# Optimization experiments

Measured on AMD Instinct MI355X. Metric: run time of the kernel, lower is better.

The kernel has to match this reference:

```python
import jax, jax.numpy as jnp
import numpy as np

_SAMPLING_EPS = 1e-05
_FP16_TINY = float(np.finfo(np.float16).tiny)  # masked_fill value used by the torch code


def _token_mask(tokens, num_seqs, vocab_size):
    # bin-count via scatter-add into width vocab+1 (padding id == vocab), then mask
    rows = jnp.arange(num_seqs)[:, None]
    counts = jnp.zeros((num_seqs, vocab_size + 1), jnp.int32).at[rows, tokens].add(1)
    return counts[:, :vocab_size] > 0


def setup_inputs() -> dict:
    key = jax.random.key(0)
    ks = jax.random.split(key, 9)
    B, V, PL, OL = 128, 128000, 2048, 256
    logits = jax.random.normal(ks[0], (B, V), dtype=jnp.float32) * 4.0
    prompt_tokens = jax.random.randint(ks[1], (B, PL), 0, V, dtype=jnp.int64)
    output_tokens = jax.random.randint(ks[2], (B, OL), 0, V, dtype=jnp.int64)
    presence_penalties = jax.random.uniform(ks[3], (B,), dtype=jnp.float32)
    frequency_penalties = jax.random.uniform(ks[4], (B,), dtype=jnp.float32)
    repetition_penalties = 1.0 + 0.3 * jax.random.uniform(ks[5], (B,), dtype=jnp.float32)
    temperature = 0.1 + 0.9 * jax.random.uniform(ks[6], (B,), dtype=jnp.float32)
    top_k = jax.random.randint(ks[7], (B,), 1, 100, dtype=jnp.int64)
    top_p = 0.5 + 0.49 * jax.random.uniform(ks[8], (B,), dtype=jnp.float32)
    return {
        "logits": logits,
        "prompt_tokens": prompt_tokens,
        "output_tokens": output_tokens,
        "presence_penalties": presence_penalties,
        "frequency_penalties": frequency_penalties,
        "repetition_penalties": repetition_penalties,
        "temperature": temperature,
        "top_k": top_k,
        "top_p": top_p,
    }


def reference(logits, prompt_tokens, output_tokens, presence_penalties,
              frequency_penalties, repetition_penalties, temperature,
              top_k, top_p):
    B, V = logits.shape
    logits = logits.astype(jnp.float32)

    # --- penalties (NOTE: torch code computes frequency counts but never applies
    # frequency_penalties; we faithfully do the same) ---
    prompt_mask = _token_mask(prompt_tokens, B, V)
    output_mask = _token_mask(output_tokens, B, V)
    pen = jnp.where(prompt_mask | output_mask, repetition_penalties[:, None], 1.0)
    logits = jnp.where(logits > 0, logits / pen, logits * pen)
    logits = logits - presence_penalties[:, None] * output_mask.astype(jnp.float32)

    # --- temperature ---
    temp = jnp.where(temperature < _SAMPLING_EPS, 1.0, temperature)
    logits = logits / temp[:, None]

    # --- top-k / top-p via ascending sort (mirrors torch implementation) ---
    idx = jnp.argsort(logits, axis=-1)                      # ascending
    ls = jnp.take_along_axis(logits, idx, axis=-1)
    thr_pos = (V - top_k.astype(jnp.int32))[:, None]
    thr = jnp.take_along_axis(ls, thr_pos, axis=-1)         # [B,1]
    ls = jnp.where(ls < thr, _FP16_TINY, ls)
    probs_sort = jax.nn.softmax(ls, axis=-1)
    csum = jnp.cumsum(probs_sort, axis=-1)
    tp_mask = csum <= (1.0 - top_p)[:, None]
    tp_mask = tp_mask.at[:, -1].set(False)
    ls = jnp.where(tp_mask, _FP16_TINY, ls)

    # unsort back to original vocab order
    rows = jnp.arange(B)[:, None]
    out_logits = jnp.zeros_like(logits).at[rows, idx].set(ls)

    probs = jax.nn.softmax(out_logits, axis=-1)
    return probs, prompt_mask, output_mask
```

## Files before the change

### kernel.cpp

```cpp
#include <hip/hip_runtime.h>
#include <math.h>

#define B   128
#define V   128000
#define WPR 4000
#define PL  2048
#define OL  256
#define BPR 25
#define ITERS 5
#define TLOC 128
#define CAP  6144
#define FP16_TINY 6.103515625e-05f

#define HBINS 4096
#define HIDX(b) ((b) + ((b) >> 4))
#define HSZ (HBINS + (HBINS >> 4))

__device__ __forceinline__ unsigned key_of(float f) {
    unsigned u = __float_as_uint(f);
    unsigned m = (unsigned)(((int)u) >> 31) | 0x80000000u;
    return u ^ m;
}
__device__ __forceinline__ float key_inv(unsigned k) {
    unsigned u = (k & 0x80000000u) ? (k ^ 0x80000000u) : ~k;
    return __uint_as_float(u);
}

__device__ __forceinline__ float xform(float x, int pm, int om,
                                       float rp, float rrp, float pres, float itt) {
#pragma clang fp contract(off)
    float m = (pm | om) ? ((x > 0.0f) ? rrp : rp) : 1.0f;
    float l = x * m;
    if (om) l = l - pres;
    return l * itt;
}

__device__ __forceinline__ unsigned wave_suffix_u(unsigned x, int lane) {
#pragma unroll
    for (int o = 1; o < 64; o <<= 1) {
        unsigned a = __shfl_down(x, o);
        if (lane + o < 64) x += a;
    }
    return x;
}
__device__ __forceinline__ unsigned wave_prefix_u(unsigned x, int lane) {
#pragma unroll
    for (int o = 1; o < 64; o <<= 1) {
        unsigned a = __shfl_up(x, o);
        if (lane >= o) x += a;
    }
    return x;
}
__device__ __forceinline__ double wave_suffix_d(double x, int lane) {
#pragma unroll
    for (int o = 1; o < 64; o <<= 1) {
        double a = __shfl_down(x, o);
        if (lane + o < 64) x += a;
    }
    return x;
}
__device__ __forceinline__ double wave_sum_d(double x) {
#pragma unroll
    for (int o = 1; o < 64; o <<= 1) x += __shfl_xor(x, o);
    return x;
}
__device__ __forceinline__ unsigned wave_sum_u(unsigned x) {
#pragma unroll
    for (int o = 1; o < 64; o <<= 1) x += __shfl_xor(x, o);
    return x;
}

__global__ __launch_bounds__(256) void k_scatter(const int* __restrict__ ptok,
                                                 const int* __restrict__ otok,
                                                 unsigned* __restrict__ bitP,
                                                 unsigned* __restrict__ bitO,
                                                 unsigned* __restrict__ cnt) {
    __shared__ unsigned mp[WPR];
    __shared__ unsigned mo[WPR];
    int r = blockIdx.x;
    int t = threadIdx.x;
    for (int i = t; i < WPR; i += 256) { mp[i] = 0u; mo[i] = 0u; }
    if (t == 0) cnt[r] = 0u;
    __syncthreads();
    const int* prow = ptok + (size_t)r * PL;
    const int* orow = otok + (size_t)r * OL;
    for (int i = t; i < PL; i += 256) {
        int tok = prow[i];
        if ((unsigned)tok < (unsigned)V) atomicOr(&mp[tok >> 5], 1u << (tok & 31));
    }
    for (int i = t; i < OL; i += 256) {
        int tok = orow[i];
        if ((unsigned)tok < (unsigned)V) atomicOr(&mo[tok >> 5], 1u << (tok & 31));
    }
    __syncthreads();
    unsigned* bpo = bitP + (size_t)r * WPR;
    unsigned* boo = bitO + (size_t)r * WPR;
    for (int i = t; i < WPR; i += 256) { bpo[i] = mp[i]; boo[i] = mo[i]; }
}

__global__ __launch_bounds__(256) void k_main(
    const float* __restrict__ logits,
    const unsigned* __restrict__ bitP, const unsigned* __restrict__ bitO,
    const float* __restrict__ rep, const float* __restrict__ pres,
    const float* __restrict__ temp,
    float* __restrict__ outPm, float* __restrict__ outOm,
    unsigned* __restrict__ cnt, unsigned long long* __restrict__ cand)
{
    __shared__ unsigned h[HSZ];
    __shared__ unsigned wsum[4];
    __shared__ int s_beta;
    __shared__ unsigned s_base;
    int r = blockIdx.y;
    int c0 = blockIdx.x * (ITERS * 1024);
    int t = threadIdx.x;
    int lane = t & 63, wid = t >> 6;
    for (int i = t; i < HSZ; i += 256) h[i] = 0u;
    __syncthreads();
    float rp = rep[r], pp = pres[r];
    float tt = temp[r]; tt = (tt < 1e-5f) ? 1.0f : tt;
    float rrp = 1.0f / rp;
    float itt = 1.0f / tt;
    const float* lrow = logits + (size_t)r * V;
    float* pmrow = outPm + (size_t)r * V;
    float* omrow = outOm + (size_t)r * V;
    const unsigned* bp = bitP + (size_t)r * WPR;
    const unsigned* bo = bitO + (size_t)r * WPR;
    uint4 kv4[ITERS];
#pragma unroll
    for (int it = 0; it < ITERS; it++) {
        int i = c0 + it * 1024 + t * 4;
        float4 x = *(const float4*)(lrow + i);
        unsigned wp = bp[i >> 5], wo = bo[i >> 5];
        int sh = i & 31;
        float xs[4] = {x.x, x.y, x.z, x.w};
        unsigned ks[4];
        float fp[4], fo[4];
#pragma unroll
        for (int j = 0; j < 4; j++) {
            int p = (wp >> (sh + j)) & 1;
            int o = (wo >> (sh + j)) & 1;
            float l = xform(xs[j], p, o, rp, rrp, pp, itt);
            unsigned key = key_of(l);
            atomicAdd(&h[HIDX(key >> 20)], 1u);
            ks[j] = key; fp[j] = (float)p; fo[j] = (float)o;
        }
        kv4[it] = make_uint4(ks[0], ks[1], ks[2], ks[3]);
        *(float4*)(pmrow + i) = make_float4(fp[0], fp[1], fp[2], fp[3]);
        *(float4*)(omrow + i) = make_float4(fo[0], fo[1], fo[2], fo[3]);
    }
    __syncthreads();
    unsigned cs = 0;
#pragma unroll
    for (int j = 0; j < 16; j++) cs += h[HIDX(t * 16 + j)];
    unsigned sfx = wave_suffix_u(cs, lane);
    if (lane == 0) wsum[wid] = sfx;
    __syncthreads();
    unsigned suf = sfx;
#pragma unroll
    for (int w2 = 0; w2 < 4; w2++) if (w2 > wid) suf += wsum[w2];
    unsigned Snext = suf - cs;
    if (suf >= TLOC && Snext < TLOC) {
        unsigned run = Snext;
        int beta = t * 16;
        for (int j = 15; j >= 0; j--) {
            run += h[HIDX(t * 16 + j)];
            if (run >= TLOC) { beta = t * 16 + j; break; }
        }
        s_beta = beta;
    }
    __syncthreads();
    unsigned beta = (unsigned)s_beta;
    unsigned myc = 0;
#pragma unroll
    for (int it = 0; it < ITERS; it++) {
        unsigned ks[4] = {kv4[it].x, kv4[it].y, kv4[it].z, kv4[it].w};
#pragma unroll
        for (int j = 0; j < 4; j++)
            if ((ks[j] >> 20) >= beta) myc++;
    }
    unsigned pfx = wave_prefix_u(myc, lane);
    if (lane == 63) wsum[wid] = pfx;
    __syncthreads();
    unsigned pv = pfx;
#pragma unroll
    for (int w2 = 0; w2 < 4; w2++) if (w2 < wid) pv += wsum[w2];
    if (t == 255) s_base = atomicAdd(&cnt[r], pv);
    __syncthreads();
    unsigned w = s_base + (pv - myc);
#pragma unroll
    for (int it = 0; it < ITERS; it++) {
        unsigned ks[4] = {kv4[it].x, kv4[it].y, kv4[it].z, kv4[it].w};
#pragma unroll
        for (int j = 0; j < 4; j++) {
            unsigned key = ks[j];
            if ((key >> 20) >= beta) {
                if (w < (unsigned)CAP) {
                    int idx = c0 + it * 1024 + t * 4 + j;
                    cand[(size_t)r * CAP + w] =
                        ((unsigned long long)key << 32) | (unsigned)idx;
                }
                w++;
            }
        }
    }
}

__global__ __launch_bounds__(256) void k_select(
    const unsigned* __restrict__ cnt, const unsigned long long* __restrict__ cand,
    const int* __restrict__ topk, const float* __restrict__ topp,
    float4* __restrict__ params, int* __restrict__ idxc,
    unsigned* __restrict__ kn, int* __restrict__ kidx, float* __restrict__ kprob)
{
    __shared__ unsigned long long list[CAP];
    __shared__ unsigned long long kv[256];
    __shared__ unsigned rh[256];
    __shared__ double wD[4];
    __shared__ unsigned wU[4];
    __shared__ unsigned s_prefix, s_krem, s_kcnt;
    int r = blockIdx.x;
    int t = threadIdx.x;
    int lane = t & 63, wid = t >> 6;
    int n = (int)min(cnt[r], (unsigned)CAP);
    const unsigned long long* crow = cand + (size_t)r * CAP;
    for (int i = t; i < n; i += 256) list[i] = crow[i];
    int k = topk[r]; k = max(1, min(k, 127));
    if (t == 0) { s_prefix = 0u; s_krem = (unsigned)k; }
    __syncthreads();
    for (int round = 3; round >= 0; round--) {
        int shift = round * 8;
        unsigned prefix = s_prefix;
        unsigned krem = s_krem;
        unsigned maskAbove = (round == 3) ? 0u : (0xFFFFFFFFu << (shift + 8));
        rh[t] = 0u;
        __syncthreads();
        for (int i = t; i < n; i += 256) {
            unsigned key = (unsigned)(list[i] >> 32);
            if ((key & maskAbove) == (prefix & maskAbove))
                atomicAdd(&rh[(key >> shift) & 255u], 1u);
        }
        __syncthreads();
        unsigned vv = rh[t];
        unsigned sfx = wave_suffix_u(vv, lane);
        if (lane == 0) wU[wid] = sfx;
        __syncthreads();
        unsigned suf = sfx;
#pragma unroll
        for (int w2 = 0; w2 < 4; w2++) if (w2 > wid) suf += wU[w2];
        unsigned Sx = suf - vv;
        if (suf >= krem && Sx < krem) {
            s_prefix = prefix | ((unsigned)t << shift);
            s_krem = krem - Sx;
        }
        __syncthreads();
    }
    unsigned thrkey = s_prefix;
    if (t == 0) s_kcnt = 0u;
    __syncthreads();
    for (int i = t; i < n; i += 256) {
        if ((unsigned)(list[i] >> 32) >= thrkey) {
            unsigned pos = atomicAdd(&s_kcnt, 1u);
            if (pos < 256u) kv[pos] = list[i];
        }
    }
    __syncthreads();
    int K = (int)min(s_kcnt, 256u);
    if (t >= K) kv[t] = 0ULL;
    __syncthreads();
    for (unsigned k2 = 2; k2 <= 256; k2 <<= 1) {
        for (unsigned j2 = k2 >> 1; j2 > 0; j2 >>= 1) {
            unsigned ixj = (unsigned)t ^ j2;
            if (ixj > (unsigned)t) {
                unsigned long long a = kv[t], b = kv[ixj];
                bool descBlock = (((unsigned)t & k2) == 0u);
                bool doSwap = descBlock ? (a < b) : (a > b);
                if (doSwap) { kv[t] = b; kv[ixj] = a; }
            }
            __syncthreads();
        }
    }
    float Mxf = key_inv((unsigned)(kv[0] >> 32));
    double MxD = (double)Mxf;
    double e_t = (t < K) ? exp((double)key_inv((unsigned)(kv[t] >> 32)) - MxD)
                         : 0.0;
    double red = wave_sum_d(e_t);
    if (lane == 0) wD[wid] = red;
    __syncthreads();
    double S = wD[0] + wD[1] + wD[2] + wD[3];
    __syncthreads();
    double sv = wave_suffix_d(e_t, lane);
    if (lane == 0) wD[wid] = sv;
    __syncthreads();
    double suf_t = sv;
#pragma unroll
    for (int w2 = 0; w2 < 4; w2++) if (w2 > wid) suf_t += wD[w2];
    double e_tinyD = exp((double)FP16_TINY - MxD);
    double Z1 = (double)(V - K) * e_tinyD + S;
    double base = (double)(V - K) * e_tinyD / Z1;
    double thresh = 1.0 - (double)topp[r];
    unsigned flag = (t >= 1 && t < K && (base + suf_t / Z1) <= thresh) ? 1u : 0u;
    unsigned fr = wave_sum_u(flag);
    if (lane == 0) wU[wid] = fr;
    __syncthreads();
    int cm = (int)(wU[0] + wU[1] + wU[2] + wU[3]);
    int ns = K - cm;
    __syncthreads();
    double e2 = (t < ns) ? e_t : 0.0;
    double r2 = wave_sum_d(e2);
    if (lane == 0) wD[wid] = r2;
    __syncthreads();
    double S2 = wD[0] + wD[1] + wD[2] + wD[3];
    unsigned bkey = (unsigned)(kv[ns - 1] >> 32);
    float v_b = key_inv(bkey);
    float tiny_e = expf(FP16_TINY - Mxf);
    double Z2 = (double)(V - ns) * (double)tiny_e + S2;
    float invZ2 = (float)(1.0 / Z2);
    if (t == 0) {
        params[r] = make_float4(v_b, Mxf, invZ2, tiny_e * invZ2);
        idxc[r] = (int)(kv[ns - 1] & 0xFFFFFFFFu);
        kn[r] = (unsigned)ns;
    }
    if (t < ns) {
        unsigned long long e = kv[t];
        unsigned key = (unsigned)(e >> 32);
        kidx[(size_t)r * 256 + t] = (int)(e & 0xFFFFFFFFu);
        kprob[(size_t)r * 256 + t] = expf(key_inv(key) - Mxf) * invZ2;
    }
}

__global__ __launch_bounds__(256) void k_final(
    const float4* __restrict__ params, const unsigned* __restrict__ kn,
    const int* __restrict__ kidx, const float* __restrict__ kprob,
    float* __restrict__ probs)
{
    int r = blockIdx.y;
    int c0 = blockIdx.x * (ITERS * 1024);
    int t = threadIdx.x;
    float ptiny = params[r].w;
    float* orow = probs + (size_t)r * V;
    float4 pv4 = make_float4(ptiny, ptiny, ptiny, ptiny);
#pragma unroll
    for (int it = 0; it < ITERS; it++) {
        int i = c0 + it * 1024 + t * 4;
        *(float4*)(orow + i) = pv4;
    }
    __syncthreads();
    int ns = (int)kn[r];
    int hi = c0 + ITERS * 1024;
    for (int i = t; i < ns; i += 256) {
        int idx = kidx[(size_t)r * 256 + i];
        if (idx >= c0 && idx < hi) orow[idx] = kprob[(size_t)r * 256 + i];
    }
}

extern "C" void kernel_launch(void* const* d_in, const int* in_sizes, int n_in,
                              void* d_out, int out_size, void* d_ws, size_t ws_size,
                              hipStream_t stream) {
    const float* logits = (const float*)d_in[0];
    const int* ptok     = (const int*)d_in[1];
    const int* otok     = (const int*)d_in[2];
    const float* pres   = (const float*)d_in[3];
    const float* rep    = (const float*)d_in[5];
    const float* temp   = (const float*)d_in[6];
    const int* topk     = (const int*)d_in[7];
    const float* topp   = (const float*)d_in[8];

    float* out_probs = (float*)d_out;
    float* out_pm = out_probs + (size_t)B * V;
    float* out_om = out_pm + (size_t)B * V;

    unsigned* ws0 = (unsigned*)d_ws;
    float4* params = (float4*)d_ws;
    int* idxc = (int*)(ws0 + 512);
    unsigned* bitP = ws0 + 768;
    unsigned* bitO = bitP + B * WPR;
    unsigned* cnt  = bitO + B * WPR;
    unsigned long long* cand =
        (unsigned long long*)(cnt + B + 64);
    unsigned* kn   = (unsigned*)(cand + (size_t)B * CAP);
    int* kidx      = (int*)(kn + B);
    float* kprob   = (float*)(kidx + B * 256);

    k_scatter<<<B, 256, 0, stream>>>(ptok, otok, bitP, bitO, cnt);

    dim3 g(BPR, B);
    k_main<<<g, 256, 0, stream>>>(logits, bitP, bitO, rep, pres, temp,
                                  out_pm, out_om, cnt, cand);
    k_select<<<B, 256, 0, stream>>>(cnt, cand, topk, topp, params, idxc,
                                    kn, kidx, kprob);
    k_final<<<g, 256, 0, stream>>>(params, kn, kidx, kprob, out_probs);
}
```

Measured before the change: 297.5 us.

## Guess candidate threshold from logit scale, fall back to histogram; rank-sort top-k

In k_main the per-block shared-memory histogram used to pick the candidate cutoff is replaced by a guessed key threshold (1.8 times 4 divided by temperature). The exact histogram path runs only when the guessed count falls outside [TLOC, GMAX]. This removes the shared atomics and several barriers on the common path, but the guess relies on the logits being roughly normal with scale 4, so other inputs take the slower fallback. In k_select the 256-element bitonic sort is replaced by an O(n) per-thread rank computation with a single scatter, which cuts many barriers at the cost of more shared-memory reads.

```diff
diff --git a/kernel.cpp b/kernel.cpp
--- a/kernel.cpp
+++ b/kernel.cpp
@@ -9,8 +9,10 @@
 #define BPR 25
 #define ITERS 5
 #define TLOC 128
+#define GMAX 240
 #define CAP  6144
 #define FP16_TINY 6.103515625e-05f
+#define QZ   1.80f
 
 #define HBINS 4096
 #define HIDX(b) ((b) + ((b) >> 4))
@@ -109,13 +111,11 @@
     __shared__ unsigned h[HSZ];
     __shared__ unsigned wsum[4];
     __shared__ int s_beta;
-    __shared__ unsigned s_base;
+    __shared__ unsigned s_base, s_total;
     int r = blockIdx.y;
     int c0 = blockIdx.x * (ITERS * 1024);
     int t = threadIdx.x;
     int lane = t & 63, wid = t >> 6;
-    for (int i = t; i < HSZ; i += 256) h[i] = 0u;
-    __syncthreads();
     float rp = rep[r], pp = pres[r];
     float tt = temp[r]; tt = (tt < 1e-5f) ? 1.0f : tt;
     float rrp = 1.0f / rp;
@@ -140,43 +140,21 @@
             int p = (wp >> (sh + j)) & 1;
             int o = (wo >> (sh + j)) & 1;
             float l = xform(xs[j], p, o, rp, rrp, pp, itt);
-            unsigned key = key_of(l);
-            atomicAdd(&h[HIDX(key >> 20)], 1u);
-            ks[j] = key; fp[j] = (float)p; fo[j] = (float)o;
+            ks[j] = key_of(l);
+            fp[j] = (float)p; fo[j] = (float)o;
         }
         kv4[it] = make_uint4(ks[0], ks[1], ks[2], ks[3]);
         *(float4*)(pmrow + i) = make_float4(fp[0], fp[1], fp[2], fp[3]);
         *(float4*)(omrow + i) = make_float4(fo[0], fo[1], fo[2], fo[3]);
     }
-    __syncthreads();
-    unsigned cs = 0;
-#pragma unroll
-    for (int j = 0; j < 16; j++) cs += h[HIDX(t * 16 + j)];
-    unsigned sfx = wave_suffix_u(cs, lane);
-    if (lane == 0) wsum[wid] = sfx;
-    __syncthreads();
-    unsigned suf = sfx;
-#pragma unroll
-    for (int w2 = 0; w2 < 4; w2++) if (w2 > wid) suf += wsum[w2];
-    unsigned Snext = suf - cs;
-    if (suf >= TLOC && Snext < TLOC) {
-        unsigned run = Snext;
-        int beta = t * 16;
-        for (int j = 15; j >= 0; j--) {
-            run += h[HIDX(t * 16 + j)];
-            if (run >= TLOC) { beta = t * 16 + j; break; }
-        }
-        s_beta = beta;
-    }
-    __syncthreads();
-    unsigned beta = (unsigned)s_beta;
+    unsigned gk = key_of(QZ * 4.0f * itt);
     unsigned myc = 0;
 #pragma unroll
     for (int it = 0; it < ITERS; it++) {
         unsigned ks[4] = {kv4[it].x, kv4[it].y, kv4[it].z, kv4[it].w};
 #pragma unroll
         for (int j = 0; j < 4; j++)
-            if ((ks[j] >> 20) >= beta) myc++;
+            if (ks[j] >= gk) myc++;
     }
     unsigned pfx = wave_prefix_u(myc, lane);
     if (lane == 63) wsum[wid] = pfx;
@@ -184,6 +162,60 @@
     unsigned pv = pfx;
 #pragma unroll
     for (int w2 = 0; w2 < 4; w2++) if (w2 < wid) pv += wsum[w2];
+    if (t == 255) s_total = pv;
+    __syncthreads();
+    unsigned total = s_total;
+    unsigned betaKey;
+    if (total >= TLOC && total <= GMAX) {
+        betaKey = gk;
+    } else {
+        for (int i = t; i < HSZ; i += 256) h[i] = 0u;
+        __syncthreads();
+#pragma unroll
+        for (int it = 0; it < ITERS; it++) {
+            unsigned ks[4] = {kv4[it].x, kv4[it].y, kv4[it].z, kv4[it].w};
+#pragma unroll
+            for (int j = 0; j < 4; j++)
+                atomicAdd(&h[HIDX(ks[j] >> 20)], 1u);
+        }
+        __syncthreads();
+        unsigned cs = 0;
+#pragma unroll
+        for (int j = 0; j < 16; j++) cs += h[HIDX(t * 16 + j)];
+        unsigned sfx = wave_suffix_u(cs, lane);
+        if (lane == 0) wsum[wid] = sfx;
+        __syncthreads();
+        unsigned suf = sfx;
+#pragma unroll
+        for (int w2 = 0; w2 < 4; w2++) if (w2 > wid) suf += wsum[w2];
+        unsigned Snext = suf - cs;
+        if (suf >= TLOC && Snext < TLOC) {
+            unsigned run = Snext;
+            int beta = t * 16;
+            for (int j = 15; j >= 0; j--) {
+                run += h[HIDX(t * 16 + j)];
+                if (run >= TLOC) { beta = t * 16 + j; break; }
+            }
+            s_beta = beta;
+        }
+        __syncthreads();
+        betaKey = ((unsigned)s_beta) << 20;
+        myc = 0;
+#pragma unroll
+        for (int it = 0; it < ITERS; it++) {
+            unsigned ks[4] = {kv4[it].x, kv4[it].y, kv4[it].z, kv4[it].w};
+#pragma unroll
+            for (int j = 0; j < 4; j++)
+                if (ks[j] >= betaKey) myc++;
+        }
+        __syncthreads();
+        pfx = wave_prefix_u(myc, lane);
+        if (lane == 63) wsum[wid] = pfx;
+        __syncthreads();
+        pv = pfx;
+#pragma unroll
+        for (int w2 = 0; w2 < 4; w2++) if (w2 < wid) pv += wsum[w2];
+    }
     if (t == 255) s_base = atomicAdd(&cnt[r], pv);
     __syncthreads();
     unsigned w = s_base + (pv - myc);
@@ -193,7 +225,7 @@
 #pragma unroll
         for (int j = 0; j < 4; j++) {
             unsigned key = ks[j];
-            if ((key >> 20) >= beta) {
+            if (key >= betaKey) {
                 if (w < (unsigned)CAP) {
                     int idx = c0 + it * 1024 + t * 4 + j;
                     cand[(size_t)r * CAP + w] =
@@ -266,18 +298,13 @@
     int K = (int)min(s_kcnt, 256u);
     if (t >= K) kv[t] = 0ULL;
     __syncthreads();
-    for (unsigned k2 = 2; k2 <= 256; k2 <<= 1) {
-        for (unsigned j2 = k2 >> 1; j2 > 0; j2 >>= 1) {
-            unsigned ixj = (unsigned)t ^ j2;
-            if (ixj > (unsigned)t) {
-                unsigned long long a = kv[t], b = kv[ixj];
-                bool descBlock = (((unsigned)t & k2) == 0u);
-                bool doSwap = descBlock ? (a < b) : (a > b);
-                if (doSwap) { kv[t] = b; kv[ixj] = a; }
-            }
-            __syncthreads();
-        }
-    }
+    unsigned long long my = kv[t];
+    int rank = 0;
+#pragma unroll 8
+    for (int i = 0; i < 256; i++) rank += (kv[i] > my) ? 1 : 0;
+    __syncthreads();
+    if (t < K) kv[rank] = my;
+    __syncthreads();
     float Mxf = key_inv((unsigned)(kv[0] >> 32));
     double MxD = (double)Mxf;
     double e_t = (t < K) ? exp((double)key_inv((unsigned)(kv[t] >> 32)) - MxD)
```

Result: no change. 296.5 us (-0.3%).
